# Kernel optimization log

Measured on AMD Instinct MI355X. Metric: run time of the kernel, lower is better.

## Reference

```python
import jax, jax.numpy as jnp
import numpy as np

# Fano-plane structure constants for the 7-dim imaginary-octonion cross product.
# Triples (i,j,k) with e_i x e_j = e_k (0-indexed), standard Cayley convention.
_FANO = [(0, 1, 2), (0, 3, 4), (0, 6, 5), (1, 3, 5), (1, 4, 6), (2, 3, 6), (2, 5, 4)]

def _structure_constants():
    f = np.zeros((7, 7, 7), dtype=np.float32)
    for i, j, k in _FANO:
        for a, b, c in ((i, j, k), (j, k, i), (k, i, j)):
            f[a, b, c] = 1.0
            f[b, a, c] = -1.0
    return jnp.asarray(f)

_F = _structure_constants()

def oct_cross(a, b):
    # a, b: [..., 7] -> imaginary-octonion cross product [..., 7]
    return jnp.einsum('ijk,...i,...j->...k', _F, a, b)

def setup_inputs() -> dict:
    key = jax.random.key(0)
    k1, k2 = jax.random.split(key)
    B, N, H = 2, 2048, 16
    o = jax.random.normal(k1, (B, N, H * 8), dtype=jnp.float32)
    invariant_mix = jax.random.normal(k2, (H, 2), dtype=jnp.float32)
    alpha = jnp.ones((H,), dtype=jnp.float32)
    beta = jnp.zeros((H,), dtype=jnp.float32)
    return {"o": o, "invariant_mix": invariant_mix, "alpha": alpha, "beta": beta}

def reference(o, invariant_mix, alpha, beta):
    B, N, D = o.shape
    H = D // 8
    oh = o.reshape(B, N, H, 8).transpose(0, 2, 1, 3)  # [B,H,N,8]
    real, imag = oh[..., :1], oh[..., 1:]             # [B,H,N,1], [B,H,N,7]
    q = k = v = imag

    k_cross_v = oct_cross(k, v)
    w = jax.nn.softmax(invariant_mix, axis=-1)        # [H,2]
    w_k = w[:, 0][None, :, None, None]
    w_t = w[:, 1][None, :, None, None]
    k_mix = w_k * k + w_t * k_cross_v                 # [B,H,N,7]

    scale = 1.0 / jnp.sqrt(jnp.asarray(7.0, o.dtype))  # SDPA default: head_dim=7
    # Both SDPA calls share Q and K_mix -> single softmax pass.
    attn = jax.nn.softmax(jnp.einsum('bhnd,bhmd->bhnm', q, k_mix) * scale, axis=-1)
    y_v = jnp.einsum('bhnm,bhmd->bhnd', attn, v)
    k_pooled = jnp.einsum('bhnm,bhmd->bhnd', attn, k)
    y_x = oct_cross(q, k_pooled)

    a = jax.nn.sigmoid(alpha)[None, :, None, None]
    b = jnp.tanh(beta)[None, :, None, None]
    imag_out = a * y_v + b * y_x                      # [B,H,N,7]

    o_out = jnp.concatenate([real, imag_out], axis=-1)  # [B,H,N,8]
    o_out = o_out.transpose(0, 2, 1, 3)                 # [B,N,H,8]
    # S7 projection: unit-normalize each octonion over its 8 components.
    norm = jnp.linalg.norm(o_out, axis=-1, keepdims=True)
    o_out = o_out / jnp.maximum(norm, 1e-12)
    return o_out.reshape(B, N, H * 8)
```

## Files before the change

kernel.cpp:

```cpp
#include <hip/hip_runtime.h>
#include <math.h>

#define B_ 2
#define N_ 2048
#define H_ 16

typedef _Float16 f16x4 __attribute__((ext_vector_type(4)));
typedef float    f32x4 __attribute__((ext_vector_type(4)));

constexpr int THREADS = 512;
constexpr int NPAIR   = N_ / 32;
constexpr int QTPB    = 16;

#if __has_builtin(__builtin_amdgcn_exp2f)
__device__ __forceinline__ float ex2(float x) { return __builtin_amdgcn_exp2f(x); }
#else
__device__ __forceinline__ float ex2(float x) { float r; asm("v_exp_f32 %0, %1" : "=v"(r) : "v"(x)); return r; }
#endif

__global__ __launch_bounds__(THREADS, 1)
void g2attn_mfma(const float* __restrict__ o, const float* __restrict__ mix,
                 const float* __restrict__ alpha, const float* __restrict__ beta,
                 float* __restrict__ out)
{
    __shared__ _Float16 sQ[NPAIR * 32 * 8];
    __shared__ _Float16 sK[NPAIR * 32 * 8];
    __shared__ _Float16 sP[NPAIR * 28 * 8];
    __shared__ float    sE[8 * 16 * 8];

    const int bh = blockIdx.y, b = bh >> 4, h = bh & (H_ - 1);
    const int tid = threadIdx.x;
    const float* obase = o + ((size_t)b * N_ * (H_ * 8)) + h * 8;

    const float m0 = mix[h * 2 + 0], m1 = mix[h * 2 + 1];
    const float wk = 1.0f / (1.0f + __expf(m1 - m0));
    const float c2 = wk * 0.5453442457918520f;

    for (int i = tid; i < N_; i += THREADS) {
        const float* src = obase + (size_t)i * (H_ * 8);
        const float4 va = *(const float4*)src;
        const float4 vb = *(const float4*)(src + 4);
        const float hd[7] = {va.y, va.z, va.w, vb.x, vb.y, vb.z, vb.w};
        const int pair = i >> 5, sub = (i >> 4) & 1, r = i & 15;
        f16x4 qlo = {(_Float16)hd[0], (_Float16)hd[1], (_Float16)hd[2], (_Float16)hd[3]};
        f16x4 qhi = {(_Float16)hd[4], (_Float16)hd[5], (_Float16)hd[6], (_Float16)1.0f};
        f16x4 klo = {(_Float16)(c2*hd[0]), (_Float16)(c2*hd[1]), (_Float16)(c2*hd[2]), (_Float16)(c2*hd[3])};
        f16x4 khi = {(_Float16)(c2*hd[4]), (_Float16)(c2*hd[5]), (_Float16)(c2*hd[6]), (_Float16)(-12.0f)};
        *(f16x4*)&sQ[((pair*32 + r)*8) + sub*4]      = qlo;
        *(f16x4*)&sQ[((pair*32 + 16 + r)*8) + sub*4] = qhi;
        *(f16x4*)&sK[((pair*32 + r)*8) + sub*4]      = klo;
        *(f16x4*)&sK[((pair*32 + 16 + r)*8) + sub*4] = khi;
        const int gw = r >> 2, jw = r & 3;
        #pragma unroll
        for (int c = 0; c < 7; ++c)
            sP[(pair*28 + gw*7 + c)*8 + sub*4 + jw] = (_Float16)hd[c];
    }
    __syncthreads();

    const int lane = tid & 63, wave = tid >> 6;
    const int cc = lane & 15, g = lane >> 4;

    const f16x4 z4   = {(_Float16)0.f, (_Float16)0.f, (_Float16)0.f, (_Float16)0.f};
    const f16x4 one4 = {(_Float16)1.f, (_Float16)1.f, (_Float16)1.f, (_Float16)1.f};
    const f32x4 zf   = {0.f, 0.f, 0.f, 0.f};

    const int t0 = blockIdx.x * QTPB + wave * 2;
    f16x4 qb0 = z4, qb1 = z4;
    if (lane < 32) {
        qb0 = *(const f16x4*)&sQ[((t0 >> 1)*32 + lane)*8 + 0];
        qb1 = *(const f16x4*)&sQ[((t0 >> 1)*32 + lane)*8 + 4];
    }

    auto loadPair = [&](int p, f16x4& a0, f16x4& a1, f16x4& b0, f16x4& b1) {
        if (lane < 32) {
            const f16x4* s = (const f16x4*)&sK[(p*32 + lane)*8];
            a0 = s[0]; a1 = s[1];
        } else { a0 = z4; a1 = z4; }
        if (cc < 7) {
            const f16x4* s = (const f16x4*)&sP[(p*28 + g*7 + cc)*8];
            b0 = s[0]; b1 = s[1];
        } else if (cc == 7) { b0 = one4; b1 = one4; }
        else { b0 = z4; b1 = z4; }
    };

    f32x4 acc0 = zf, acc1 = zf;
    f16x4 ka0, ka1, pa0, pa1;
    loadPair(0, ka0, ka1, pa0, pa1);

    for (int p = 0; p < NPAIR; ++p) {
        f16x4 nk0 = z4, nk1 = z4, np0 = z4, np1 = z4;
        if (p + 1 < NPAIR) loadPair(p + 1, nk0, nk1, np0, np1);

        f32x4 s0 = __builtin_amdgcn_mfma_f32_16x16x16f16(ka0, qb0, zf, 0, 0, 0);
        f32x4 s1 = __builtin_amdgcn_mfma_f32_16x16x16f16(ka0, qb1, zf, 0, 0, 0);
        f32x4 s2 = __builtin_amdgcn_mfma_f32_16x16x16f16(ka1, qb0, zf, 0, 0, 0);
        f32x4 s3 = __builtin_amdgcn_mfma_f32_16x16x16f16(ka1, qb1, zf, 0, 0, 0);

        f16x4 pb0, pb1, pb2, pb3;
        #define MKPB(S, PB) { \
            float e0 = ex2(S[0]), e1 = ex2(S[1]), e2 = ex2(S[2]), e3 = ex2(S[3]); \
            auto lo = __builtin_amdgcn_cvt_pkrtz(e0, e1); \
            auto hi = __builtin_amdgcn_cvt_pkrtz(e2, e3); \
            PB[0] = (_Float16)lo[0]; PB[1] = (_Float16)lo[1]; \
            PB[2] = (_Float16)hi[0]; PB[3] = (_Float16)hi[1]; }
        MKPB(s0, pb0) MKPB(s1, pb1) MKPB(s2, pb2) MKPB(s3, pb3)
        #undef MKPB

        acc0 = __builtin_amdgcn_mfma_f32_16x16x16f16(pa0, pb0, acc0, 0, 0, 0);
        acc1 = __builtin_amdgcn_mfma_f32_16x16x16f16(pa0, pb1, acc1, 0, 0, 0);
        acc0 = __builtin_amdgcn_mfma_f32_16x16x16f16(pa1, pb2, acc0, 0, 0, 0);
        acc1 = __builtin_amdgcn_mfma_f32_16x16x16f16(pa1, pb3, acc1, 0, 0, 0);

        ka0 = nk0; ka1 = nk1; pa0 = np0; pa1 = np1;
    }

    const float sa = 1.0f / (1.0f + __expf(-alpha[h]));
    const float tb = tanhf(beta[h]);

    #pragma unroll
    for (int which = 0; which < 2; ++which) {
        __syncthreads();
        const f32x4 a = which ? acc1 : acc0;
        if (lane < 32) {
            #pragma unroll
            for (int r = 0; r < 4; ++r)
                sE[(wave*16 + cc)*8 + g*4 + r] = a[r];
        }
        __syncthreads();
        if (lane < 16) {
            const float* e = &sE[(wave*16 + lane)*8];
            const float invl = 1.0f / e[7];
            float ya[7];
            #pragma unroll
            for (int d = 0; d < 7; ++d) ya[d] = e[d] * invl;

            const int q = (t0 + which)*16 + lane;
            const float* src = obase + (size_t)q * (H_ * 8);
            const float4 va = *(const float4*)src;
            const float4 vb = *(const float4*)(src + 4);
            const float realv = va.x;
            const float qf[7] = {va.y, va.z, va.w, vb.x, vb.y, vb.z, vb.w};

            float xa[7] = {0.f, 0.f, 0.f, 0.f, 0.f, 0.f, 0.f};
            const int TR[7][3] = {{0,1,2},{0,3,4},{0,6,5},{1,3,5},{1,4,6},{2,3,6},{2,5,4}};
            #pragma unroll
            for (int t = 0; t < 7; ++t) {
                const int i = TR[t][0], j = TR[t][1], k = TR[t][2];
                xa[k] += qf[i]*ya[j] - qf[j]*ya[i];
                xa[i] += qf[j]*ya[k] - qf[k]*ya[j];
                xa[j] += qf[k]*ya[i] - qf[i]*ya[k];
            }

            float im[7], nsq = realv * realv;
            #pragma unroll
            for (int d = 0; d < 7; ++d) {
                im[d] = sa*ya[d] + tb*xa[d];
                nsq = fmaf(im[d], im[d], nsq);
            }
            const float inv = 1.0f / fmaxf(sqrtf(nsq), 1e-12f);

            float* dst = out + ((size_t)(b*N_ + q)*H_ + h)*8;
            float4 oA = {realv*inv, im[0]*inv, im[1]*inv, im[2]*inv};
            float4 oB = {im[3]*inv, im[4]*inv, im[5]*inv, im[6]*inv};
            *(float4*)dst       = oA;
            *(float4*)(dst + 4) = oB;
        }
    }
}

extern "C" void kernel_launch(void* const* d_in, const int* in_sizes, int n_in,
                              void* d_out, int out_size, void* d_ws, size_t ws_size,
                              hipStream_t stream) {
    const float* o     = (const float*)d_in[0];
    const float* mix   = (const float*)d_in[1];
    const float* alpha = (const float*)d_in[2];
    const float* beta  = (const float*)d_in[3];
    float* out = (float*)d_out;

    dim3 grid(N_ / (QTPB * 16), B_ * H_);
    g2attn_mfma<<<grid, THREADS, 0, stream>>>(o, mix, alpha, beta, out);
}
```

Baseline: 83.41 us.

## Split key dimension across blocks and reduce partials in a separate finalize kernel

The attention kernel now splits keys into four chunks per block and writes unnormalized partial sums (numerator and denominator) to workspace. A second kernel sums the partials, normalizes, applies the octonion cross term and the S7 projection. Each block stages only its key chunk in LDS, and Q fragments are loaded straight from global memory. This is meant to raise block count and occupancy and cut redundant full-sequence staging, at the cost of an extra launch and workspace traffic. Because the exponent uses a fixed offset rather than a running max, summing partials stays valid.

```diff
diff --git a/kernel.cpp b/kernel.cpp
--- a/kernel.cpp
+++ b/kernel.cpp
@@ -9,53 +9,45 @@
 typedef float    f32x4 __attribute__((ext_vector_type(4)));
 
 constexpr int THREADS = 512;
-constexpr int NPAIR   = N_ / 32;
-constexpr int QTPB    = 16;
-
-#if __has_builtin(__builtin_amdgcn_exp2f)
+constexpr int KSPLIT  = 4;
+constexpr int PPB     = 16;
+constexpr int QCH     = 256;
+
 __device__ __forceinline__ float ex2(float x) { return __builtin_amdgcn_exp2f(x); }
-#else
-__device__ __forceinline__ float ex2(float x) { float r; asm("v_exp_f32 %0, %1" : "=v"(r) : "v"(x)); return r; }
-#endif
-
-__global__ __launch_bounds__(THREADS, 1)
-void g2attn_mfma(const float* __restrict__ o, const float* __restrict__ mix,
-                 const float* __restrict__ alpha, const float* __restrict__ beta,
-                 float* __restrict__ out)
+
+__global__ __launch_bounds__(THREADS, 8)
+void g2attn_main(const float* __restrict__ o, const float* __restrict__ mix,
+                 float* __restrict__ ws)
 {
-    __shared__ _Float16 sQ[NPAIR * 32 * 8];
-    __shared__ _Float16 sK[NPAIR * 32 * 8];
-    __shared__ _Float16 sP[NPAIR * 28 * 8];
-    __shared__ float    sE[8 * 16 * 8];
+    __shared__ _Float16 sK[PPB * 32 * 8];
+    __shared__ _Float16 sP[PPB * 28 * 8];
 
     const int bh = blockIdx.y, b = bh >> 4, h = bh & (H_ - 1);
+    const int qc = blockIdx.x >> 2, kh = blockIdx.x & 3;
     const int tid = threadIdx.x;
-    const float* obase = o + ((size_t)b * N_ * (H_ * 8)) + h * 8;
+    const float* obase = o + ((size_t)b * N_ * 128) + h * 8;
 
     const float m0 = mix[h * 2 + 0], m1 = mix[h * 2 + 1];
     const float wk = 1.0f / (1.0f + __expf(m1 - m0));
     const float c2 = wk * 0.5453442457918520f;
 
-    for (int i = tid; i < N_; i += THREADS) {
-        const float* src = obase + (size_t)i * (H_ * 8);
+    {
+        const int i = tid;
+        const int krow = kh * 512 + i;
+        const float* src = obase + (size_t)krow * 128;
         const float4 va = *(const float4*)src;
         const float4 vb = *(const float4*)(src + 4);
         const float hd[7] = {va.y, va.z, va.w, vb.x, vb.y, vb.z, vb.w};
-        const int pair = i >> 5, sub = (i >> 4) & 1, r = i & 15;
-        f16x4 qlo = {(_Float16)hd[0], (_Float16)hd[1], (_Float16)hd[2], (_Float16)hd[3]};
-        f16x4 qhi = {(_Float16)hd[4], (_Float16)hd[5], (_Float16)hd[6], (_Float16)1.0f};
+        const int kp = i >> 5, sub = (i >> 4) & 1, r = i & 15;
         f16x4 klo = {(_Float16)(c2*hd[0]), (_Float16)(c2*hd[1]), (_Float16)(c2*hd[2]), (_Float16)(c2*hd[3])};
         f16x4 khi = {(_Float16)(c2*hd[4]), (_Float16)(c2*hd[5]), (_Float16)(c2*hd[6]), (_Float16)(-12.0f)};
-        *(f16x4*)&sQ[((pair*32 + r)*8) + sub*4]      = qlo;
-        *(f16x4*)&sQ[((pair*32 + 16 + r)*8) + sub*4] = qhi;
-        *(f16x4*)&sK[((pair*32 + r)*8) + sub*4]      = klo;
-        *(f16x4*)&sK[((pair*32 + 16 + r)*8) + sub*4] = khi;
+        *(f16x4*)&sK[((kp*32 + r)*8) + sub*4]      = klo;
+        *(f16x4*)&sK[((kp*32 + 16 + r)*8) + sub*4] = khi;
         const int gw = r >> 2, jw = r & 3;
         #pragma unroll
         for (int c = 0; c < 7; ++c)
-            sP[(pair*28 + gw*7 + c)*8 + sub*4 + jw] = (_Float16)hd[c];
-    }
-    __syncthreads();
+            sP[(kp*28 + gw*7 + c)*8 + sub*4 + jw] = (_Float16)hd[c];
+    }
 
     const int lane = tid & 63, wave = tid >> 6;
     const int cc = lane & 15, g = lane >> 4;
@@ -64,12 +56,24 @@
     const f16x4 one4 = {(_Float16)1.f, (_Float16)1.f, (_Float16)1.f, (_Float16)1.f};
     const f32x4 zf   = {0.f, 0.f, 0.f, 0.f};
 
-    const int t0 = blockIdx.x * QTPB + wave * 2;
     f16x4 qb0 = z4, qb1 = z4;
     if (lane < 32) {
-        qb0 = *(const f16x4*)&sQ[((t0 >> 1)*32 + lane)*8 + 0];
-        qb1 = *(const f16x4*)&sQ[((t0 >> 1)*32 + lane)*8 + 4];
-    }
+        const int q0 = qc * QCH + wave * 32 + cc;
+        const float* rA = obase + (size_t)q0 * 128;
+        const float* rB = rA + 16 * 128;
+        const float4 a0 = *(const float4*)rA;
+        const float4 a1 = *(const float4*)(rA + 4);
+        const float4 b0 = *(const float4*)rB;
+        const float4 b1 = *(const float4*)(rB + 4);
+        if (g == 0) {
+            qb0 = (f16x4){(_Float16)a0.y, (_Float16)a0.z, (_Float16)a0.w, (_Float16)a1.x};
+            qb1 = (f16x4){(_Float16)b0.y, (_Float16)b0.z, (_Float16)b0.w, (_Float16)b1.x};
+        } else {
+            qb0 = (f16x4){(_Float16)a1.y, (_Float16)a1.z, (_Float16)a1.w, (_Float16)1.0f};
+            qb1 = (f16x4){(_Float16)b1.y, (_Float16)b1.z, (_Float16)b1.w, (_Float16)1.0f};
+        }
+    }
+    __syncthreads();
 
     auto loadPair = [&](int p, f16x4& a0, f16x4& a1, f16x4& b0, f16x4& b1) {
         if (lane < 32) {
@@ -87,85 +91,103 @@
     f16x4 ka0, ka1, pa0, pa1;
     loadPair(0, ka0, ka1, pa0, pa1);
 
-    for (int p = 0; p < NPAIR; ++p) {
-        f16x4 nk0 = z4, nk1 = z4, np0 = z4, np1 = z4;
-        if (p + 1 < NPAIR) loadPair(p + 1, nk0, nk1, np0, np1);
+    #define MKPB(S, PB) { \
+        float e0 = ex2(S[0]), e1 = ex2(S[1]), e2 = ex2(S[2]), e3 = ex2(S[3]); \
+        auto lo = __builtin_amdgcn_cvt_pkrtz(e0, e1); \
+        auto hi = __builtin_amdgcn_cvt_pkrtz(e2, e3); \
+        PB[0] = (_Float16)lo[0]; PB[1] = (_Float16)lo[1]; \
+        PB[2] = (_Float16)hi[0]; PB[3] = (_Float16)hi[1]; }
+
+    for (int p = 0; p < PPB; ++p) {
+        f16x4 nk0, nk1, np0, np1;
+        loadPair((p + 1) & (PPB - 1), nk0, nk1, np0, np1);
 
         f32x4 s0 = __builtin_amdgcn_mfma_f32_16x16x16f16(ka0, qb0, zf, 0, 0, 0);
         f32x4 s1 = __builtin_amdgcn_mfma_f32_16x16x16f16(ka0, qb1, zf, 0, 0, 0);
+        f16x4 pb0, pb1;
+        MKPB(s0, pb0) MKPB(s1, pb1)
+        acc0 = __builtin_amdgcn_mfma_f32_16x16x16f16(pa0, pb0, acc0, 0, 0, 0);
+        acc1 = __builtin_amdgcn_mfma_f32_16x16x16f16(pa0, pb1, acc1, 0, 0, 0);
+
         f32x4 s2 = __builtin_amdgcn_mfma_f32_16x16x16f16(ka1, qb0, zf, 0, 0, 0);
         f32x4 s3 = __builtin_amdgcn_mfma_f32_16x16x16f16(ka1, qb1, zf, 0, 0, 0);
-
-        f16x4 pb0, pb1, pb2, pb3;
-        #define MKPB(S, PB) { \
-            float e0 = ex2(S[0]), e1 = ex2(S[1]), e2 = ex2(S[2]), e3 = ex2(S[3]); \
-            auto lo = __builtin_amdgcn_cvt_pkrtz(e0, e1); \
-            auto hi = __builtin_amdgcn_cvt_pkrtz(e2, e3); \
-            PB[0] = (_Float16)lo[0]; PB[1] = (_Float16)lo[1]; \
-            PB[2] = (_Float16)hi[0]; PB[3] = (_Float16)hi[1]; }
-        MKPB(s0, pb0) MKPB(s1, pb1) MKPB(s2, pb2) MKPB(s3, pb3)
-        #undef MKPB
-
-        acc0 = __builtin_amdgcn_mfma_f32_16x16x16f16(pa0, pb0, acc0, 0, 0, 0);
-        acc1 = __builtin_amdgcn_mfma_f32_16x16x16f16(pa0, pb1, acc1, 0, 0, 0);
+        f16x4 pb2, pb3;
+        MKPB(s2, pb2) MKPB(s3, pb3)
         acc0 = __builtin_amdgcn_mfma_f32_16x16x16f16(pa1, pb2, acc0, 0, 0, 0);
         acc1 = __builtin_amdgcn_mfma_f32_16x16x16f16(pa1, pb3, acc1, 0, 0, 0);
 
         ka0 = nk0; ka1 = nk1; pa0 = np0; pa1 = np1;
     }
+    #undef MKPB
+
+    if (lane < 32) {
+        const int q0 = qc * QCH + wave * 32 + cc;
+        float* w0 = ws + ((((size_t)bh * N_ + q0) * 4 + kh) * 8) + g * 4;
+        float* w1 = ws + ((((size_t)bh * N_ + q0 + 16) * 4 + kh) * 8) + g * 4;
+        *(f32x4*)w0 = acc0;
+        *(f32x4*)w1 = acc1;
+    }
+}
+
+__global__ __launch_bounds__(256, 8)
+void g2attn_fin(const float* __restrict__ o, const float* __restrict__ ws,
+                const float* __restrict__ alpha, const float* __restrict__ beta,
+                float* __restrict__ out)
+{
+    const int gid = blockIdx.x * 256 + threadIdx.x;
+    const int h = gid & (H_ - 1);
+    const int bq = gid >> 4;
+    const int b = bq >> 11;
+    const int bh = b * H_ + h;
+    const int q = bq & (N_ - 1);
+
+    const float* p = ws + (((size_t)bh * N_ + q) * 4) * 8;
+    float e[8] = {0.f, 0.f, 0.f, 0.f, 0.f, 0.f, 0.f, 0.f};
+    #pragma unroll
+    for (int kh = 0; kh < 4; ++kh) {
+        const float4 a = *(const float4*)(p + kh * 8);
+        const float4 c = *(const float4*)(p + kh * 8 + 4);
+        e[0] += a.x; e[1] += a.y; e[2] += a.z; e[3] += a.w;
+        e[4] += c.x; e[5] += c.y; e[6] += c.z; e[7] += c.w;
+    }
+    const float invl = 1.0f / e[7];
+
+    const float* src = o + (size_t)bq * 128 + h * 8;
+    const float4 va = *(const float4*)src;
+    const float4 vb = *(const float4*)(src + 4);
+    const float realv = va.x;
+    const float qf[7] = {va.y, va.z, va.w, vb.x, vb.y, vb.z, vb.w};
+
+    float ya[7];
+    #pragma unroll
+    for (int d = 0; d < 7; ++d) ya[d] = e[d] * invl;
+
+    float xa[7] = {0.f, 0.f, 0.f, 0.f, 0.f, 0.f, 0.f};
+    const int TR[7][3] = {{0,1,2},{0,3,4},{0,6,5},{1,3,5},{1,4,6},{2,3,6},{2,5,4}};
+    #pragma unroll
+    for (int t = 0; t < 7; ++t) {
+        const int i = TR[t][0], j = TR[t][1], k = TR[t][2];
+        xa[k] += qf[i]*ya[j] - qf[j]*ya[i];
+        xa[i] += qf[j]*ya[k] - qf[k]*ya[j];
+        xa[j] += qf[k]*ya[i] - qf[i]*ya[k];
+    }
 
     const float sa = 1.0f / (1.0f + __expf(-alpha[h]));
     const float tb = tanhf(beta[h]);
 
-    #pragma unroll
-    for (int which = 0; which < 2; ++which) {
-        __syncthreads();
-        const f32x4 a = which ? acc1 : acc0;
-        if (lane < 32) {
-            #pragma unroll
-            for (int r = 0; r < 4; ++r)
-                sE[(wave*16 + cc)*8 + g*4 + r] = a[r];
-        }
-        __syncthreads();
-        if (lane < 16) {
-            const float* e = &sE[(wave*16 + lane)*8];
-            const float invl = 1.0f / e[7];
-            float ya[7];
-            #pragma unroll
-            for (int d = 0; d < 7; ++d) ya[d] = e[d] * invl;
-
-            const int q = (t0 + which)*16 + lane;
-            const float* src = obase + (size_t)q * (H_ * 8);
-            const float4 va = *(const float4*)src;
-            const float4 vb = *(const float4*)(src + 4);
-            const float realv = va.x;
-            const float qf[7] = {va.y, va.z, va.w, vb.x, vb.y, vb.z, vb.w};
-
-            float xa[7] = {0.f, 0.f, 0.f, 0.f, 0.f, 0.f, 0.f};
-            const int TR[7][3] = {{0,1,2},{0,3,4},{0,6,5},{1,3,5},{1,4,6},{2,3,6},{2,5,4}};
-            #pragma unroll
-            for (int t = 0; t < 7; ++t) {
-                const int i = TR[t][0], j = TR[t][1], k = TR[t][2];
-                xa[k] += qf[i]*ya[j] - qf[j]*ya[i];
-                xa[i] += qf[j]*ya[k] - qf[k]*ya[j];
-                xa[j] += qf[k]*ya[i] - qf[i]*ya[k];
-            }
-
-            float im[7], nsq = realv * realv;
-            #pragma unroll
-            for (int d = 0; d < 7; ++d) {
-                im[d] = sa*ya[d] + tb*xa[d];
-                nsq = fmaf(im[d], im[d], nsq);
-            }
-            const float inv = 1.0f / fmaxf(sqrtf(nsq), 1e-12f);
-
-            float* dst = out + ((size_t)(b*N_ + q)*H_ + h)*8;
-            float4 oA = {realv*inv, im[0]*inv, im[1]*inv, im[2]*inv};
-            float4 oB = {im[3]*inv, im[4]*inv, im[5]*inv, im[6]*inv};
-            *(float4*)dst       = oA;
-            *(float4*)(dst + 4) = oB;
-        }
-    }
+    float im[7], nsq = realv * realv;
+    #pragma unroll
+    for (int d = 0; d < 7; ++d) {
+        im[d] = sa*ya[d] + tb*xa[d];
+        nsq = fmaf(im[d], im[d], nsq);
+    }
+    const float inv = 1.0f / fmaxf(sqrtf(nsq), 1e-12f);
+
+    float* dst = out + (size_t)bq * 128 + h * 8;
+    float4 oA = {realv*inv, im[0]*inv, im[1]*inv, im[2]*inv};
+    float4 oB = {im[3]*inv, im[4]*inv, im[5]*inv, im[6]*inv};
+    *(float4*)dst       = oA;
+    *(float4*)(dst + 4) = oB;
 }
 
 extern "C" void kernel_launch(void* const* d_in, const int* in_sizes, int n_in,
@@ -176,7 +198,11 @@
     const float* alpha = (const float*)d_in[2];
     const float* beta  = (const float*)d_in[3];
     float* out = (float*)d_out;
-
-    dim3 grid(N_ / (QTPB * 16), B_ * H_);
-    g2attn_mfma<<<grid, THREADS, 0, stream>>>(o, mix, alpha, beta, out);
+    float* ws  = (float*)d_ws;
+
+    dim3 grid1((N_ / QCH) * KSPLIT, B_ * H_);
+    g2attn_main<<<grid1, THREADS, 0, stream>>>(o, mix, ws);
+
+    dim3 grid2((B_ * N_ * H_) / 256);
+    g2attn_fin<<<grid2, 256, 0, stream>>>(o, ws, alpha, beta, out);
 }
```

After: 83.58 us. No clear change (+0.2%).
